# Kernel tuning notes

Hardware: AMD Instinct MI355X
Metric: run time of the kernel (lower is better)

## Reference

```python
import jax, jax.numpy as jnp
import numpy as np

HEADS = 16

def _conv1(x, W, b):
    # pointwise Conv1d: x (B, Cin, L), W (Cout, Cin), b (Cout,)
    return jnp.einsum('oi,bil->bol', W, x) + b[None, :, None]


def setup_inputs() -> dict:
    key = jax.random.key(0)
    ks = jax.random.split(key, 5)
    B, S, L = 8, 1024, 1024
    sc = 1.0 / np.sqrt(S)
    return {
        'x': jax.random.normal(ks[0], (B, S, L), jnp.float32),
        'y': jax.random.normal(ks[1], (B, S, L), jnp.float32),
        'W_k': jax.random.normal(ks[2], (S, S), jnp.float32) * sc,
        'b_k': jnp.zeros((S,), jnp.float32),
        'W_q': jax.random.normal(ks[3], (S, S), jnp.float32) * sc,
        'b_q': jnp.zeros((S,), jnp.float32),
        'W_p': jax.random.normal(ks[4], (S, S), jnp.float32) * sc,
        'b_p': jnp.zeros((S,), jnp.float32),
    }


def reference(x, y, W_k, b_k, W_q, b_q, W_p, b_p):
    B, S, L = x.shape
    H = HEADS
    d = S // H
    keys = _conv1(x, W_k, b_k).reshape(B * H, d, L)
    queries = _conv1(y, W_q, b_q).reshape(B * H, d, L)
    # scores = keys^T @ queries : (B*H, L, L)
    scores = jnp.einsum('bdl,bdm->blm', keys, queries)
    # faithful to original: seqlen ** 1 / 2 == seqlen / 2 (not sqrt)
    attn = jax.nn.softmax(scores / (L / 2.0), axis=-1)
    xs = x.reshape(B * H, d, L)
    out = jnp.einsum('bdl,blm->bdm', xs, attn)  # (B*H, d, L)
    out = out.reshape(B, S, L)
    return _conv1(out, W_p, b_p)
```

## Files before the change

### kernel.cpp

```cpp
#include <hip/hip_runtime.h>
#include <hip/hip_bf16.h>

typedef unsigned short u16;
typedef u16 u16x8 __attribute__((ext_vector_type(8)));
typedef u16 u16x4 __attribute__((ext_vector_type(4)));
typedef __bf16 bf16x8 __attribute__((ext_vector_type(8)));
typedef float f32x4 __attribute__((ext_vector_type(4)));

#define INV512 0.001953125f

__device__ __forceinline__ u16 f2bf(float f) {
  __hip_bfloat16 h = __float2bfloat16(f);
  return __builtin_bit_cast(u16, h);
}

__device__ __forceinline__ void gload16(const void* g, void* l) {
  __builtin_amdgcn_global_load_lds((__attribute__((address_space(1))) void*)(g),
                                   (__attribute__((address_space(3))) void*)(l), 16, 0, 0);
}

__global__ __launch_bounds__(256) void convert_xpose(const float* __restrict__ src,
                                                     u16* __restrict__ natdst,
                                                     u16* __restrict__ trdst) {
  __shared__ float t[64][65];
  const int b = blockIdx.z;
  const int i0 = blockIdx.y * 64;
  const int l0 = blockIdx.x * 64;
  const int tid = threadIdx.x;
  const float* sbase = src + ((size_t)b * 1024 + i0) * 1024 + l0;
#pragma unroll
  for (int e = 0; e < 4; ++e) {
    const int idx = e * 256 + tid;
    const int r = idx >> 4, c4 = (idx & 15) * 4;
    float4 v = *(const float4*)(sbase + (size_t)r * 1024 + c4);
    t[r][c4 + 0] = v.x; t[r][c4 + 1] = v.y; t[r][c4 + 2] = v.z; t[r][c4 + 3] = v.w;
  }
  __syncthreads();
  if (natdst) {
    u16* nb = natdst + ((size_t)b * 1024 + i0) * 1024 + l0;
#pragma unroll
    for (int e = 0; e < 2; ++e) {
      const int g = e * 256 + tid;
      const int r = g >> 3, c8 = (g & 7) * 8;
      u16x8 o;
#pragma unroll
      for (int j = 0; j < 8; ++j) o[j] = f2bf(t[r][c8 + j]);
      *(u16x8*)(nb + (size_t)r * 1024 + (c8 ^ ((r & 7) << 3))) = o;
    }
  }
  {
    u16* tb = trdst + ((size_t)b * 1024 + l0) * 1024 + i0;
#pragma unroll
    for (int e = 0; e < 2; ++e) {
      const int g = e * 256 + tid;
      const int lr = g >> 3, i8 = (g & 7) * 8;
      u16x8 o;
#pragma unroll
      for (int j = 0; j < 8; ++j) o[j] = f2bf(t[i8 + j][lr]);
      *(u16x8*)(tb + (size_t)lr * 1024 + (i8 ^ ((lr & 7) << 3))) = o;
    }
  }
}

__global__ __launch_bounds__(256) void convert_w(const float* __restrict__ w0, const float* __restrict__ w1,
                                                 const float* __restrict__ w2, u16* __restrict__ d0,
                                                 u16* __restrict__ d1, u16* __restrict__ d2) {
  const float* s;
  u16* d;
  if (blockIdx.y == 0) { s = w0; d = d0; }
  else if (blockIdx.y == 1) { s = w1; d = d1; }
  else { s = w2; d = d2; }
  const int g = blockIdx.x * 256 + threadIdx.x;
  const int o = g >> 7;
  const int i8 = (g & 127) * 8;
  float4 a = *(const float4*)(s + (size_t)o * 1024 + i8);
  float4 bv = *(const float4*)(s + (size_t)o * 1024 + i8 + 4);
  u16x8 u;
  u[0] = f2bf(a.x); u[1] = f2bf(a.y); u[2] = f2bf(a.z); u[3] = f2bf(a.w);
  u[4] = f2bf(bv.x); u[5] = f2bf(bv.y); u[6] = f2bf(bv.z); u[7] = f2bf(bv.w);
  const int is = (i8 & ~63) | ((i8 & 63) ^ ((o & 7) << 3));
  *(u16x8*)(d + (size_t)o * 1024 + is) = u;
}

template <bool OUTBF16, bool BIASROW>
__global__ __launch_bounds__(256) void gemm_tn(const u16* __restrict__ A, const u16* __restrict__ Bm,
                                               const float* __restrict__ bias, void* __restrict__ Cout,
                                               size_t sA, size_t sB, size_t sC) {
  __shared__ u16 Al[128 * 64];
  __shared__ u16 Bl[128 * 64];
  const int b = blockIdx.z;
  const int m0 = blockIdx.y * 128, n0 = blockIdx.x * 128;
  const int tid = threadIdx.x, lane = tid & 63, w = tid >> 6;
  const int wm = (w >> 1) * 64, wn = (w & 1) * 64;
  const u16* Ab = A + (size_t)b * sA + (size_t)m0 * 1024;
  const u16* Bb = Bm + (size_t)b * sB + (size_t)n0 * 1024;
  f32x4 acc[4][4] = {};
  for (int kt = 0; kt < 16; ++kt) {
    const int k0 = kt * 64;
#pragma unroll
    for (int p = 0; p < 4; ++p) {
      const int e = p * 2048 + tid * 8;
      const int r = e >> 6, c = e & 63;
      gload16(Ab + (size_t)r * 1024 + k0 + c, &Al[e]);
      gload16(Bb + (size_t)r * 1024 + k0 + c, &Bl[e]);
    }
    __syncthreads();
#pragma unroll
    for (int ks = 0; ks < 2; ++ks) {
      const int kk = ks * 32 + (lane >> 4) * 8;
      bf16x8 af[4], bfr[4];
#pragma unroll
      for (int i = 0; i < 4; ++i) {
        const int ra = wm + i * 16 + (lane & 15);
        af[i] = *(const bf16x8*)&Al[ra * 64 + (kk ^ ((ra & 7) << 3))];
        const int rb = wn + i * 16 + (lane & 15);
        bfr[i] = *(const bf16x8*)&Bl[rb * 64 + (kk ^ ((rb & 7) << 3))];
      }
#pragma unroll
      for (int i = 0; i < 4; ++i)
#pragma unroll
        for (int j = 0; j < 4; ++j)
          acc[i][j] = __builtin_amdgcn_mfma_f32_16x16x32_bf16(af[i], bfr[j], acc[i][j], 0, 0, 0);
    }
    __syncthreads();
  }
  const int g4 = (lane >> 4) * 4, ln = lane & 15;
#pragma unroll
  for (int i = 0; i < 4; ++i) {
#pragma unroll
    for (int j = 0; j < 4; ++j) {
#pragma unroll
      for (int jj = 0; jj < 4; ++jj) {
        const int r = m0 + wm + i * 16 + g4 + jj;
        const int c = n0 + wn + j * 16 + ln;
        const float v = acc[i][j][jj] + (BIASROW ? bias[r] : bias[c]);
        if (OUTBF16) {
          u16* C = (u16*)Cout + (size_t)b * sC;
          const int cs = (c & ~63) | ((c & 63) ^ ((r & 7) << 3));
          C[(size_t)r * 1024 + cs] = f2bf(v);
        } else {
          float* C = (float*)Cout + (size_t)b * sC;
          C[(size_t)r * 1024 + c] = v;
        }
      }
    }
  }
}

__global__ __launch_bounds__(256) void pass_a(const u16* __restrict__ keysT,
                                              const u16* __restrict__ queriesT,
                                              float* __restrict__ invZ) {
  __shared__ u16 Kl[128 * 64];
  __shared__ u16 Ql[128 * 64];
  const int bh = blockIdx.y, b = bh >> 4, h = bh & 15;
  const int l0 = blockIdx.x * 128;
  const int tid = threadIdx.x, lane = tid & 63, w = tid >> 6;
  const u16* Kg = keysT + ((size_t)b * 1024 + l0) * 1024 + h * 64;
  const u16* Qg = queriesT + (size_t)b * 1024 * 1024 + h * 64;
#pragma unroll
  for (int p = 0; p < 4; ++p) {
    const int e = p * 2048 + tid * 8, r = e >> 6, c = e & 63;
    gload16(Kg + (size_t)r * 1024 + c, &Kl[e]);
  }
  float psum[2][4] = {};
  for (int mt = 0; mt < 8; ++mt) {
#pragma unroll
    for (int p = 0; p < 4; ++p) {
      const int e = p * 2048 + tid * 8, r = e >> 6, c = e & 63;
      gload16(Qg + (size_t)(mt * 128 + r) * 1024 + c, &Ql[e]);
    }
    __syncthreads();
    bf16x8 af[2][2];
#pragma unroll
    for (int mf = 0; mf < 2; ++mf)
#pragma unroll
      for (int ks = 0; ks < 2; ++ks) {
        const int ra = w * 32 + mf * 16 + (lane & 15);
        const int kk = ks * 32 + (lane >> 4) * 8;
        af[mf][ks] = *(const bf16x8*)&Kl[ra * 64 + (kk ^ ((ra & 7) << 3))];
      }
#pragma unroll
    for (int nf = 0; nf < 8; ++nf) {
      bf16x8 bq[2];
#pragma unroll
      for (int ks = 0; ks < 2; ++ks) {
        const int rb = nf * 16 + (lane & 15);
        const int kk = ks * 32 + (lane >> 4) * 8;
        bq[ks] = *(const bf16x8*)&Ql[rb * 64 + (kk ^ ((rb & 7) << 3))];
      }
#pragma unroll
      for (int mf = 0; mf < 2; ++mf) {
        f32x4 s = {0.f, 0.f, 0.f, 0.f};
        s = __builtin_amdgcn_mfma_f32_16x16x32_bf16(af[mf][0], bq[0], s, 0, 0, 0);
        s = __builtin_amdgcn_mfma_f32_16x16x32_bf16(af[mf][1], bq[1], s, 0, 0, 0);
#pragma unroll
        for (int jj = 0; jj < 4; ++jj) psum[mf][jj] += __expf(s[jj] * INV512);
      }
    }
    __syncthreads();
  }
#pragma unroll
  for (int mf = 0; mf < 2; ++mf)
#pragma unroll
    for (int jj = 0; jj < 4; ++jj) {
      float v = psum[mf][jj];
      v += __shfl_xor(v, 1); v += __shfl_xor(v, 2); v += __shfl_xor(v, 4); v += __shfl_xor(v, 8);
      if ((lane & 15) == 0)
        invZ[(size_t)bh * 1024 + l0 + w * 32 + mf * 16 + (lane >> 4) * 4 + jj] = 1.0f / v;
    }
}

__global__ __launch_bounds__(256) void pass_b(const u16* __restrict__ keysT,
                                              const u16* __restrict__ queriesT,
                                              const u16* __restrict__ xb,
                                              const float* __restrict__ invZ,
                                              u16* __restrict__ outT) {
  __shared__ u16 Ql[128 * 64];
  __shared__ u16 Kl[64 * 64];
  __shared__ u16 Xl[64 * 64];
  __shared__ u16 El[128 * 72];
  __shared__ float Zl[64];
  const int bh = blockIdx.y, b = bh >> 4, h = bh & 15;
  const int m0 = blockIdx.x * 128;
  const int tid = threadIdx.x, lane = tid & 63, w = tid >> 6;
  const u16* Qg = queriesT + ((size_t)b * 1024 + m0) * 1024 + h * 64;
  const u16* Kg = keysT + (size_t)b * 1024 * 1024 + h * 64;
  const u16* Xg = xb + (size_t)(b * 1024 + h * 64) * 1024;
#pragma unroll
  for (int p = 0; p < 4; ++p) {
    const int e = p * 2048 + tid * 8, r = e >> 6, c = e & 63;
    gload16(Qg + (size_t)r * 1024 + c, &Ql[e]);
  }
  f32x4 acc[2][4] = {};
  for (int lt = 0; lt < 16; ++lt) {
    const int l0 = lt * 64;
#pragma unroll
    for (int p = 0; p < 2; ++p) {
      const int e = p * 2048 + tid * 8, r = e >> 6, c = e & 63;
      gload16(Kg + (size_t)(l0 + r) * 1024 + c, &Kl[e]);
      gload16(Xg + (size_t)r * 1024 + l0 + c, &Xl[e]);
    }
    if (tid < 64) Zl[tid] = invZ[(size_t)bh * 1024 + l0 + tid];
    __syncthreads();
    bf16x8 bq[2][2];
#pragma unroll
    for (int nf = 0; nf < 2; ++nf)
#pragma unroll
      for (int ks = 0; ks < 2; ++ks) {
        const int rb = w * 32 + nf * 16 + (lane & 15);
        const int kk = ks * 32 + (lane >> 4) * 8;
        bq[nf][ks] = *(const bf16x8*)&Ql[rb * 64 + (kk ^ ((rb & 7) << 3))];
      }
#pragma unroll
    for (int lf = 0; lf < 4; ++lf) {
      bf16x8 ak[2];
#pragma unroll
      for (int ks = 0; ks < 2; ++ks) {
        const int ra = lf * 16 + (lane & 15);
        const int kk = ks * 32 + (lane >> 4) * 8;
        ak[ks] = *(const bf16x8*)&Kl[ra * 64 + (kk ^ ((ra & 7) << 3))];
      }
      const int lb = lf * 16 + (lane >> 4) * 4;
#pragma unroll
      for (int nf = 0; nf < 2; ++nf) {
        f32x4 s = {0.f, 0.f, 0.f, 0.f};
        s = __builtin_amdgcn_mfma_f32_16x16x32_bf16(ak[0], bq[nf][0], s, 0, 0, 0);
        s = __builtin_amdgcn_mfma_f32_16x16x32_bf16(ak[1], bq[nf][1], s, 0, 0, 0);
        const int m = w * 32 + nf * 16 + (lane & 15);
        u16x4 ev;
#pragma unroll
        for (int jj = 0; jj < 4; ++jj)
          ev[jj] = f2bf(__expf(s[jj] * INV512) * Zl[lb + jj]);
        *(u16x4*)&El[m * 72 + lb] = ev;
      }
    }
    bf16x8 ae[2][2];
#pragma unroll
    for (int mf = 0; mf < 2; ++mf)
#pragma unroll
      for (int ks = 0; ks < 2; ++ks) {
        const int ra = w * 32 + mf * 16 + (lane & 15);
        const int kk = ks * 32 + (lane >> 4) * 8;
        ae[mf][ks] = *(const bf16x8*)&El[ra * 72 + kk];
      }
#pragma unroll
    for (int df = 0; df < 4; ++df) {
      bf16x8 bx[2];
#pragma unroll
      for (int ks = 0; ks < 2; ++ks) {
        const int rb = df * 16 + (lane & 15);
        const int kk = ks * 32 + (lane >> 4) * 8;
        bx[ks] = *(const bf16x8*)&Xl[rb * 64 + (kk ^ ((rb & 7) << 3))];
      }
#pragma unroll
      for (int mf = 0; mf < 2; ++mf) {
        acc[mf][df] = __builtin_amdgcn_mfma_f32_16x16x32_bf16(ae[mf][0], bx[0], acc[mf][df], 0, 0, 0);
        acc[mf][df] = __builtin_amdgcn_mfma_f32_16x16x32_bf16(ae[mf][1], bx[1], acc[mf][df], 0, 0, 0);
      }
    }
    __syncthreads();
  }
  u16* Og = outT + ((size_t)b * 1024 + m0) * 1024 + h * 64;
#pragma unroll
  for (int mf = 0; mf < 2; ++mf)
#pragma unroll
    for (int df = 0; df < 4; ++df)
#pragma unroll
      for (int jj = 0; jj < 4; ++jj) {
        const int m = w * 32 + mf * 16 + (lane >> 4) * 4 + jj;
        const int dd = df * 16 + (lane & 15);
        Og[(size_t)m * 1024 + (dd ^ ((m & 7) << 3))] = f2bf(acc[mf][df][jj]);
      }
}

extern "C" void kernel_launch(void* const* d_in, const int* in_sizes, int n_in,
                              void* d_out, int out_size, void* d_ws, size_t ws_size,
                              hipStream_t stream) {
  (void)in_sizes; (void)n_in; (void)out_size; (void)ws_size;
  const float* x  = (const float*)d_in[0];
  const float* y  = (const float*)d_in[1];
  const float* Wk = (const float*)d_in[2];
  const float* bk = (const float*)d_in[3];
  const float* Wq = (const float*)d_in[4];
  const float* bq = (const float*)d_in[5];
  const float* Wp = (const float*)d_in[6];
  const float* bp = (const float*)d_in[7];
  float* out = (float*)d_out;

  char* ws = (char*)d_ws;
  size_t off = 0;
  auto wsalloc = [&](size_t bytes) -> void* {
    void* p = ws + off;
    off += (bytes + 255) & ~(size_t)255;
    return p;
  };
  const size_t T16 = (size_t)8 * 1024 * 1024 * 2;
  u16* xb       = (u16*)wsalloc(T16);
  u16* xT       = (u16*)wsalloc(T16);
  u16* yT       = (u16*)wsalloc(T16);
  u16* Wk16     = (u16*)wsalloc((size_t)1024 * 1024 * 2);
  u16* Wq16     = (u16*)wsalloc((size_t)1024 * 1024 * 2);
  u16* Wp16     = (u16*)wsalloc((size_t)1024 * 1024 * 2);
  u16* keysT    = (u16*)wsalloc(T16);
  u16* queriesT = (u16*)wsalloc(T16);
  u16* outT     = (u16*)wsalloc(T16);
  float* invZ   = (float*)wsalloc((size_t)128 * 1024 * 4);

  const dim3 blk(256);
  convert_xpose<<<dim3(16, 16, 8), blk, 0, stream>>>(x, xb, xT);
  convert_xpose<<<dim3(16, 16, 8), blk, 0, stream>>>(y, nullptr, yT);
  convert_w<<<dim3(512, 3), blk, 0, stream>>>(Wk, Wq, Wp, Wk16, Wq16, Wp16);
  gemm_tn<true, false><<<dim3(8, 8, 8), blk, 0, stream>>>(xT, Wk16, bk, keysT,
                                                          1048576, 0, 1048576);
  gemm_tn<true, false><<<dim3(8, 8, 8), blk, 0, stream>>>(yT, Wq16, bq, queriesT,
                                                          1048576, 0, 1048576);
  pass_a<<<dim3(8, 128), blk, 0, stream>>>(keysT, queriesT, invZ);
  pass_b<<<dim3(8, 128), blk, 0, stream>>>(keysT, queriesT, xb, invZ, outT);
  gemm_tn<false, true><<<dim3(8, 8, 8), blk, 0, stream>>>(Wp16, outT, bp, out,
                                                          0, 1048576, 1048576);
}
```

Measured before the change: 305.2 us.

## Double-buffer attention passes, remap blocks per XCD, fold normalizer into exp2

```diff
diff --git a/kernel.cpp b/kernel.cpp
--- a/kernel.cpp
+++ b/kernel.cpp
@@ -7,7 +7,7 @@
 typedef __bf16 bf16x8 __attribute__((ext_vector_type(8)));
 typedef float f32x4 __attribute__((ext_vector_type(4)));
 
-#define INV512 0.001953125f
+#define C2 0.0028177637517362567f
 
 __device__ __forceinline__ u16 f2bf(float f) {
   __hip_bfloat16 h = __float2bfloat16(f);
@@ -88,8 +88,10 @@
                                                size_t sA, size_t sB, size_t sC) {
   __shared__ u16 Al[128 * 64];
   __shared__ u16 Bl[128 * 64];
-  const int b = blockIdx.z;
-  const int m0 = blockIdx.y * 128, n0 = blockIdx.x * 128;
+  const int bid = blockIdx.x;
+  const int flat = (bid & 7) * 64 + (bid >> 3);
+  const int b = flat >> 6;
+  const int m0 = ((flat >> 3) & 7) * 128, n0 = (flat & 7) * 128;
   const int tid = threadIdx.x, lane = tid & 63, w = tid >> 6;
   const int wm = (w >> 1) * 64, wn = (w & 1) * 64;
   const u16* Ab = A + (size_t)b * sA + (size_t)m0 * 1024;
@@ -149,36 +151,43 @@
 
 __global__ __launch_bounds__(256) void pass_a(const u16* __restrict__ keysT,
                                               const u16* __restrict__ queriesT,
-                                              float* __restrict__ invZ) {
-  __shared__ u16 Kl[128 * 64];
-  __shared__ u16 Ql[128 * 64];
-  const int bh = blockIdx.y, b = bh >> 4, h = bh & 15;
-  const int l0 = blockIdx.x * 128;
+                                              float* __restrict__ zlog) {
+  __shared__ u16 Qd[2][128 * 64];
+  const int bid = blockIdx.x;
+  const int flat = (bid & 7) * 128 + (bid >> 3);
+  const int bh = flat >> 3;
+  const int l0 = (flat & 7) * 128;
+  const int b = bh >> 4, h = bh & 15;
   const int tid = threadIdx.x, lane = tid & 63, w = tid >> 6;
   const u16* Kg = keysT + ((size_t)b * 1024 + l0) * 1024 + h * 64;
   const u16* Qg = queriesT + (size_t)b * 1024 * 1024 + h * 64;
 #pragma unroll
   for (int p = 0; p < 4; ++p) {
     const int e = p * 2048 + tid * 8, r = e >> 6, c = e & 63;
-    gload16(Kg + (size_t)r * 1024 + c, &Kl[e]);
-  }
+    gload16(Kg + (size_t)r * 1024 + c, &Qd[1][e]);
+    gload16(Qg + (size_t)r * 1024 + c, &Qd[0][e]);
+  }
+  __syncthreads();
+  bf16x8 af[2][2];
+#pragma unroll
+  for (int mf = 0; mf < 2; ++mf)
+#pragma unroll
+    for (int ks = 0; ks < 2; ++ks) {
+      const int ra = w * 32 + mf * 16 + (lane & 15);
+      const int kk = ks * 32 + (lane >> 4) * 8;
+      af[mf][ks] = *(const bf16x8*)&Qd[1][ra * 64 + (kk ^ ((ra & 7) << 3))];
+    }
+  __syncthreads();
   float psum[2][4] = {};
+  int cur = 0;
   for (int mt = 0; mt < 8; ++mt) {
-#pragma unroll
-    for (int p = 0; p < 4; ++p) {
-      const int e = p * 2048 + tid * 8, r = e >> 6, c = e & 63;
-      gload16(Qg + (size_t)(mt * 128 + r) * 1024 + c, &Ql[e]);
-    }
-    __syncthreads();
-    bf16x8 af[2][2];
-#pragma unroll
-    for (int mf = 0; mf < 2; ++mf)
-#pragma unroll
-      for (int ks = 0; ks < 2; ++ks) {
-        const int ra = w * 32 + mf * 16 + (lane & 15);
-        const int kk = ks * 32 + (lane >> 4) * 8;
-        af[mf][ks] = *(const bf16x8*)&Kl[ra * 64 + (kk ^ ((ra & 7) << 3))];
-      }
+    if (mt < 7) {
+#pragma unroll
+      for (int p = 0; p < 4; ++p) {
+        const int e = p * 2048 + tid * 8, r = e >> 6, c = e & 63;
+        gload16(Qg + (size_t)((mt + 1) * 128 + r) * 1024 + c, &Qd[cur ^ 1][e]);
+      }
+    }
 #pragma unroll
     for (int nf = 0; nf < 8; ++nf) {
       bf16x8 bq[2];
@@ -186,7 +195,7 @@
       for (int ks = 0; ks < 2; ++ks) {
         const int rb = nf * 16 + (lane & 15);
         const int kk = ks * 32 + (lane >> 4) * 8;
-        bq[ks] = *(const bf16x8*)&Ql[rb * 64 + (kk ^ ((rb & 7) << 3))];
+        bq[ks] = *(const bf16x8*)&Qd[cur][rb * 64 + (kk ^ ((rb & 7) << 3))];
       }
 #pragma unroll
       for (int mf = 0; mf < 2; ++mf) {
@@ -194,10 +203,12 @@
         s = __builtin_amdgcn_mfma_f32_16x16x32_bf16(af[mf][0], bq[0], s, 0, 0, 0);
         s = __builtin_amdgcn_mfma_f32_16x16x32_bf16(af[mf][1], bq[1], s, 0, 0, 0);
 #pragma unroll
-        for (int jj = 0; jj < 4; ++jj) psum[mf][jj] += __expf(s[jj] * INV512);
+        for (int jj = 0; jj < 4; ++jj)
+          psum[mf][jj] += __builtin_amdgcn_exp2f(s[jj] * C2);
       }
     }
     __syncthreads();
+    cur ^= 1;
   }
 #pragma unroll
   for (int mf = 0; mf < 2; ++mf)
@@ -206,22 +217,24 @@
       float v = psum[mf][jj];
       v += __shfl_xor(v, 1); v += __shfl_xor(v, 2); v += __shfl_xor(v, 4); v += __shfl_xor(v, 8);
       if ((lane & 15) == 0)
-        invZ[(size_t)bh * 1024 + l0 + w * 32 + mf * 16 + (lane >> 4) * 4 + jj] = 1.0f / v;
+        zlog[(size_t)bh * 1024 + l0 + w * 32 + mf * 16 + (lane >> 4) * 4 + jj] =
+            -__builtin_amdgcn_logf(v);
     }
 }
 
 __global__ __launch_bounds__(256) void pass_b(const u16* __restrict__ keysT,
                                               const u16* __restrict__ queriesT,
                                               const u16* __restrict__ xb,
-                                              const float* __restrict__ invZ,
+                                              const float* __restrict__ zlog,
                                               u16* __restrict__ outT) {
-  __shared__ u16 Ql[128 * 64];
-  __shared__ u16 Kl[64 * 64];
-  __shared__ u16 Xl[64 * 64];
-  __shared__ u16 El[128 * 72];
-  __shared__ float Zl[64];
-  const int bh = blockIdx.y, b = bh >> 4, h = bh & 15;
-  const int m0 = blockIdx.x * 128;
+  __shared__ u16 KX[2][2][4096];
+  __shared__ u16 El[128 * 64];
+  __shared__ float Zl[2][64];
+  const int bid = blockIdx.x;
+  const int flat = (bid & 7) * 128 + (bid >> 3);
+  const int bh = flat >> 3;
+  const int m0 = (flat & 7) * 128;
+  const int b = bh >> 4, h = bh & 15;
   const int tid = threadIdx.x, lane = tid & 63, w = tid >> 6;
   const u16* Qg = queriesT + ((size_t)b * 1024 + m0) * 1024 + h * 64;
   const u16* Kg = keysT + (size_t)b * 1024 * 1024 + h * 64;
@@ -229,28 +242,40 @@
 #pragma unroll
   for (int p = 0; p < 4; ++p) {
     const int e = p * 2048 + tid * 8, r = e >> 6, c = e & 63;
-    gload16(Qg + (size_t)r * 1024 + c, &Ql[e]);
-  }
+    gload16(Qg + (size_t)r * 1024 + c, &El[e]);
+  }
+#pragma unroll
+  for (int p = 0; p < 2; ++p) {
+    const int e = p * 2048 + tid * 8, r = e >> 6, c = e & 63;
+    gload16(Kg + (size_t)r * 1024 + c, &KX[0][0][e]);
+    gload16(Xg + (size_t)r * 1024 + c, &KX[0][1][e]);
+  }
+  if (tid < 64) Zl[0][tid] = zlog[(size_t)bh * 1024 + tid];
+  __syncthreads();
+  bf16x8 bq[2][2];
+#pragma unroll
+  for (int nf = 0; nf < 2; ++nf)
+#pragma unroll
+    for (int ks = 0; ks < 2; ++ks) {
+      const int rb = w * 32 + nf * 16 + (lane & 15);
+      const int kk = ks * 32 + (lane >> 4) * 8;
+      bq[nf][ks] = *(const bf16x8*)&El[rb * 64 + (kk ^ ((rb & 7) << 3))];
+    }
   f32x4 acc[2][4] = {};
+  int cur = 0;
   for (int lt = 0; lt < 16; ++lt) {
-    const int l0 = lt * 64;
-#pragma unroll
-    for (int p = 0; p < 2; ++p) {
-      const int e = p * 2048 + tid * 8, r = e >> 6, c = e & 63;
-      gload16(Kg + (size_t)(l0 + r) * 1024 + c, &Kl[e]);
-      gload16(Xg + (size_t)r * 1024 + l0 + c, &Xl[e]);
-    }
-    if (tid < 64) Zl[tid] = invZ[(size_t)bh * 1024 + l0 + tid];
-    __syncthreads();
-    bf16x8 bq[2][2];
-#pragma unroll
-    for (int nf = 0; nf < 2; ++nf)
-#pragma unroll
-      for (int ks = 0; ks < 2; ++ks) {
-        const int rb = w * 32 + nf * 16 + (lane & 15);
-        const int kk = ks * 32 + (lane >> 4) * 8;
-        bq[nf][ks] = *(const bf16x8*)&Ql[rb * 64 + (kk ^ ((rb & 7) << 3))];
-      }
+    if (lt < 15) {
+      const int l1 = (lt + 1) * 64;
+#pragma unroll
+      for (int p = 0; p < 2; ++p) {
+        const int e = p * 2048 + tid * 8, r = e >> 6, c = e & 63;
+        gload16(Kg + (size_t)(l1 + r) * 1024 + c, &KX[cur ^ 1][0][e]);
+        gload16(Xg + (size_t)r * 1024 + l1 + c, &KX[cur ^ 1][1][e]);
+      }
+      if (tid < 64) Zl[cur ^ 1][tid] = zlog[(size_t)bh * 1024 + l1 + tid];
+    }
+    const u16* Kl = KX[cur][0];
+    const u16* Xl = KX[cur][1];
 #pragma unroll
     for (int lf = 0; lf < 4; ++lf) {
       bf16x8 ak[2];
@@ -270,8 +295,8 @@
         u16x4 ev;
 #pragma unroll
         for (int jj = 0; jj < 4; ++jj)
-          ev[jj] = f2bf(__expf(s[jj] * INV512) * Zl[lb + jj]);
-        *(u16x4*)&El[m * 72 + lb] = ev;
+          ev[jj] = f2bf(__builtin_amdgcn_exp2f(fmaf(s[jj], C2, Zl[cur][lb + jj])));
+        *(u16x4*)&El[m * 64 + (lb ^ ((m & 7) << 3))] = ev;
       }
     }
     bf16x8 ae[2][2];
@@ -281,7 +306,7 @@
       for (int ks = 0; ks < 2; ++ks) {
         const int ra = w * 32 + mf * 16 + (lane & 15);
         const int kk = ks * 32 + (lane >> 4) * 8;
-        ae[mf][ks] = *(const bf16x8*)&El[ra * 72 + kk];
+        ae[mf][ks] = *(const bf16x8*)&El[ra * 64 + (kk ^ ((ra & 7) << 3))];
       }
 #pragma unroll
     for (int df = 0; df < 4; ++df) {
@@ -299,6 +324,7 @@
       }
     }
     __syncthreads();
+    cur ^= 1;
   }
   u16* Og = outT + ((size_t)b * 1024 + m0) * 1024 + h * 64;
 #pragma unroll
@@ -344,18 +370,18 @@
   u16* keysT    = (u16*)wsalloc(T16);
   u16* queriesT = (u16*)wsalloc(T16);
   u16* outT     = (u16*)wsalloc(T16);
-  float* invZ   = (float*)wsalloc((size_t)128 * 1024 * 4);
+  float* zlog   = (float*)wsalloc((size_t)128 * 1024 * 4);
 
   const dim3 blk(256);
   convert_xpose<<<dim3(16, 16, 8), blk, 0, stream>>>(x, xb, xT);
   convert_xpose<<<dim3(16, 16, 8), blk, 0, stream>>>(y, nullptr, yT);
   convert_w<<<dim3(512, 3), blk, 0, stream>>>(Wk, Wq, Wp, Wk16, Wq16, Wp16);
-  gemm_tn<true, false><<<dim3(8, 8, 8), blk, 0, stream>>>(xT, Wk16, bk, keysT,
-                                                          1048576, 0, 1048576);
-  gemm_tn<true, false><<<dim3(8, 8, 8), blk, 0, stream>>>(yT, Wq16, bq, queriesT,
-                                                          1048576, 0, 1048576);
-  pass_a<<<dim3(8, 128), blk, 0, stream>>>(keysT, queriesT, invZ);
-  pass_b<<<dim3(8, 128), blk, 0, stream>>>(keysT, queriesT, xb, invZ, outT);
-  gemm_tn<false, true><<<dim3(8, 8, 8), blk, 0, stream>>>(Wp16, outT, bp, out,
-                                                          0, 1048576, 1048576);
-}
+  gemm_tn<true, false><<<dim3(512), blk, 0, stream>>>(xT, Wk16, bk, keysT,
+                                                      1048576, 0, 1048576);
+  gemm_tn<true, false><<<dim3(512), blk, 0, stream>>>(yT, Wq16, bq, queriesT,
+                                                      1048576, 0, 1048576);
+  pass_a<<<dim3(1024), blk, 0, stream>>>(keysT, queriesT, zlog);
+  pass_b<<<dim3(1024), blk, 0, stream>>>(keysT, queriesT, xb, zlog, outT);
+  gemm_tn<false, true><<<dim3(512), blk, 0, stream>>>(Wp16, outT, bp, out,
+                                                      0, 1048576, 1048576);
+}
```

New measurement: 290.0 us. 1.05x faster.
